# Optimization experiments

Hardware: AMD Instinct MI355X
Metric: run time of the kernel (lower is better)

The kernel has to match this reference:

```python
import jax, jax.numpy as jnp
import numpy as np

B, S, D = 2, 2048, 1024
H, HD = 16, 64          # num_heads, head_dim
K = 32                  # JL n_components


def setup_inputs() -> dict:
    key = jax.random.key(0)
    k1, k2, k3, k4 = jax.random.split(key, 4)
    return {
        "hidden_states": jax.random.normal(k1, (B, S, D), dtype=jnp.float32),
        "W_attn": jax.random.normal(k2, (D, 3 * D), dtype=jnp.float32) * 0.02,
        "b_attn": jnp.zeros((3 * D,), dtype=jnp.float32),
        "S_proj": jax.random.normal(k3, (K, HD), dtype=jnp.float32) / np.sqrt(K),
        "W_proj": jax.random.normal(k4, (D, D), dtype=jnp.float32) * 0.02,
        "b_proj": jnp.zeros((D,), dtype=jnp.float32),
    }


def reference(hidden_states, W_attn, b_attn, S_proj, W_proj, b_proj):
    b, s, d = hidden_states.shape
    # GPT2 Conv1D: x @ W + b, then split into q,k,v
    qkv = hidden_states @ W_attn + b_attn            # [B,S,3D]
    q, k, v = jnp.split(qkv, 3, axis=-1)
    # split heads -> [B,H,S,HD]
    def split_heads(x):
        return x.reshape(b, s, H, HD).transpose(0, 2, 1, 3)
    q = split_heads(q) @ S_proj.T                    # [B,H,S,K] JL-reduced
    k = split_heads(k) @ S_proj.T                    # [B,H,S,K]
    v = split_heads(v)                               # [B,H,S,HD]
    # naive attention: scale by sqrt(value head_dim) per GPT2 _attn
    scores = jnp.einsum("bhqk,bhsk->bhqs", q, k) / jnp.sqrt(
        jnp.asarray(HD, dtype=v.dtype))              # [B,H,S,S]
    causal = jnp.tril(jnp.ones((s, s), dtype=bool))
    mask_value = jnp.finfo(scores.dtype).min
    scores = jnp.where(causal, scores, mask_value)
    attn = jax.nn.softmax(scores, axis=-1)
    out = jnp.einsum("bhqs,bhsd->bhqd", attn, v)     # [B,H,S,HD]
    out = out.transpose(0, 2, 1, 3).reshape(b, s, d)  # merge heads
    return out @ W_proj + b_proj
```

## Files before the change

### kernel.cpp

```cpp
#include <hip/hip_runtime.h>
#include <hip/hip_bf16.h>
#include <stdint.h>

#define B_ 2
#define S_ 2048
#define D_ 1024
#define H_ 16
#define HD_ 64
#define KJL 32
#define N3 3072
#define N2 2048

typedef __attribute__((ext_vector_type(8))) __bf16 bf16x8;
typedef __attribute__((ext_vector_type(4))) float floatx4;
typedef __attribute__((ext_vector_type(4))) short short4v;
typedef __attribute__((ext_vector_type(2))) unsigned int uint2v;

__device__ __forceinline__ unsigned short f2b(float x) {
  union { float f; unsigned u; } v; v.f = x;
  unsigned r = v.u + 0x7fffu + ((v.u >> 16) & 1u);
  return (unsigned short)(r >> 16);
}

__device__ __forceinline__ unsigned int pkbf(float lo, float hi) {
  union { float f; unsigned u; } a, b;
  a.f = lo; b.f = hi;
  return __builtin_amdgcn_perm(b.u + 0x8000u, a.u + 0x8000u, 0x07060302u);
}

__device__ __forceinline__ void async16(const void* g, void* l) {
  __builtin_amdgcn_global_load_lds((__attribute__((address_space(1))) void*)(g),
                                   (__attribute__((address_space(3))) void*)(l),
                                   16, 0, 0);
}

__global__ __launch_bounds__(256)
void prep_kernel(const float* __restrict__ hidden, unsigned short* __restrict__ hB,
                 const float* __restrict__ W_attn, const float* __restrict__ b_attn,
                 const float* __restrict__ Sp, const float* __restrict__ W_proj,
                 unsigned short* __restrict__ Bt2, unsigned short* __restrict__ WpT,
                 float* __restrict__ bias2) {
  __shared__ float shmem[2048];
  const int bid = blockIdx.x;
  const int tid = threadIdx.x;

  if (bid < 512) {
    const int n4 = (B_ * S_ * D_) / 4;
    int i = bid * 256 + tid;
    for (; i < n4; i += 512 * 256) {
      float4 v = *(const float4*)(hidden + 4 * (size_t)i);
      short4v o = {(short)f2b(v.x), (short)f2b(v.y), (short)f2b(v.z), (short)f2b(v.w)};
      *(short4v*)(hB + 4 * (size_t)i) = o;
    }
  } else if (bid < 2560) {
    const float* in;
    unsigned short* out;
    int Cs, local;
    if (bid < 1536) { local = bid - 512;  in = W_attn + 2048; out = Bt2 + 1024 * 1024; Cs = N3; }
    else            { local = bid - 1536; in = W_proj;        out = WpT;               Cs = D_; }
    float (*t)[33] = (float(*)[33])shmem;
    int c0 = (local & 31) * 32, r0 = (local >> 5) * 32;
    int tx = tid & 31, ty = tid >> 5;
    for (int j = 0; j < 32; j += 8)
      t[ty + j][tx] = in[(size_t)(r0 + ty + j) * Cs + c0 + tx];
    __syncthreads();
    for (int j = 0; j < 32; j += 8)
      out[(size_t)(c0 + ty + j) * D_ + r0 + tx] = f2b(t[tx][ty + j]);
  } else {
    const int lb = bid - 2560;
    const int part = lb >> 6;
    const int h = (lb >> 2) & 15;
    const int dc = lb & 3;
    for (int i = tid; i < 32 * 64; i += 256) shmem[i] = Sp[i];
    __syncthreads();
    const float scale = part ? 1.0f : 0.125f * 1.44269504f;
    const int d = dc * 256 + tid;
    float w[64];
    const float* src = W_attn + (size_t)d * N3 + part * D_ + h * 64;
    for (int j = 0; j < 16; ++j) {
      float4 v = *(const float4*)&src[j * 4];
      w[j * 4 + 0] = v.x; w[j * 4 + 1] = v.y; w[j * 4 + 2] = v.z; w[j * 4 + 3] = v.w;
    }
    const int nbase = part * 512 + h * 32;
    for (int kjl = 0; kjl < 32; ++kjl) {
      float acc = 0.f;
      for (int hd = 0; hd < 64; ++hd) acc += w[hd] * shmem[kjl * 64 + hd];
      Bt2[(size_t)(nbase + kjl) * D_ + d] = f2b(acc * scale);
    }
    if (dc == 0 && tid < 32) {
      float acc = 0.f;
      for (int hd = 0; hd < 64; ++hd) acc += b_attn[part * D_ + h * 64 + hd] * shmem[tid * 64 + hd];
      bias2[nbase + tid] = acc * scale;
    }
  }
}

__global__ __launch_bounds__(256, 2)
void qkv2_gemm_kernel(const unsigned short* __restrict__ A,
                      const unsigned short* __restrict__ Bt,
                      const float* __restrict__ b_attn,
                      const float* __restrict__ bias2,
                      unsigned short* __restrict__ Qjl,
                      unsigned short* __restrict__ Kjl,
                      unsigned short* __restrict__ Vc) {
  __shared__ __align__(16) unsigned short As[2][128 * 32];
  __shared__ __align__(16) unsigned short Bs[2][128 * 32];
  const int tid = threadIdx.x;
  const int lane = tid & 63, wv = tid >> 6;
  const int quad = lane >> 4, col = lane & 15;
  const int wm = wv >> 1, wn = wv & 1;
  const int m0 = blockIdx.y * 128, n0 = blockIdx.x * 128;

  floatx4 acc[4][4] = {};

  for (int kk = 0; kk < D_; kk += 64) {
    for (int it = 0; it < 4; ++it) {
      int c = it * 256 + tid;
      int ks = c >> 9, row = (c >> 2) & 127, kc = c & 3;
      async16(A + (size_t)(m0 + row) * D_ + kk + ks * 32 + kc * 8,
              (unsigned short*)As + c * 8);
    }
    for (int it = 0; it < 4; ++it) {
      int c = it * 256 + tid;
      int ks = c >> 9, row = (c >> 2) & 127, kc = c & 3;
      async16(Bt + (size_t)(n0 + row) * D_ + kk + ks * 32 + kc * 8,
              (unsigned short*)Bs + c * 8);
    }
    asm volatile("s_waitcnt vmcnt(0)" ::: "memory");
    __syncthreads();
    for (int ks = 0; ks < 2; ++ks) {
      bf16x8 af[4], bfr[4];
      for (int mt = 0; mt < 4; ++mt)
        af[mt] = *(const bf16x8*)&As[ks][(wm * 64 + mt * 16 + col) * 32 + quad * 8];
      for (int nt = 0; nt < 4; ++nt)
        bfr[nt] = *(const bf16x8*)&Bs[ks][(wn * 64 + nt * 16 + col) * 32 + quad * 8];
      for (int mt = 0; mt < 4; ++mt)
        for (int nt = 0; nt < 4; ++nt)
          acc[mt][nt] = __builtin_amdgcn_mfma_f32_16x16x32_bf16(
              af[mt], bfr[nt], acc[mt][nt], 0, 0, 0);
    }
    __syncthreads();
  }

  const int pq = n0 >> 9;
  for (int mt = 0; mt < 4; ++mt) {
    int gm0 = m0 + wm * 64 + mt * 16 + quad * 4;
    int b = gm0 >> 11, s = gm0 & (S_ - 1);
    for (int nt = 0; nt < 4; ++nt) {
      int gn = n0 + wn * 64 + nt * 16 + col;
      if (pq >= 2) {
        int vcol = gn - 1024;
        float bs = b_attn[2048 + vcol];
        int h = vcol >> 6, hd = vcol & 63;
        short4v vv;
        for (int i = 0; i < 4; ++i)
          vv[i] = (short)f2b(acc[mt][nt][i] + bs);
        size_t idx = ((((size_t)(b * H_ + h) * 64 + (s >> 5)) * 64 + hd) * 32 + (s & 31));
        *(short4v*)&Vc[idx] = vv;
      } else {
        float bs = bias2[gn];
        int gl = gn & 511;
        int h = gl >> 5, kjl = gl & 31;
        unsigned short* dst = pq ? Kjl : Qjl;
        size_t base = ((size_t)(b * H_ + h) * S_ + s) * KJL + kjl;
        for (int i = 0; i < 4; ++i)
          dst[base + (size_t)i * KJL] = f2b(acc[mt][nt][i] + bs);
      }
    }
  }
}

__global__ __launch_bounds__(256, 2)
void attn_kernel(const unsigned short* __restrict__ Qjl,
                 const unsigned short* __restrict__ Kjl,
                 const unsigned short* __restrict__ Vc,
                 unsigned short* __restrict__ AO) {
  __shared__ __align__(16) unsigned short Kb[2][4096];
  __shared__ __align__(16) unsigned short Vb[2][8192];
  __shared__ __align__(16) unsigned short Ps[4][2048];
  const int tid = threadIdx.x;
  const int lane = tid & 63, wv = tid >> 6;
  const int quad = lane >> 4, l15 = lane & 15;

  const int blk = blockIdx.x;
  const int bh = blk & 31;
  const int v = blk >> 5;
  const int b = bh >> 4, h = bh & 15;

  const unsigned short* Kg = Kjl + (size_t)bh * S_ * KJL;
  const unsigned short* Vg = Vc + (size_t)bh * (64 * 64 * 32);

  char* Pw = (char*)&Ps[wv][0];
  const int pswz = l15 << 4;
  const floatx4 zz = {0.f, 0.f, 0.f, 0.f};

#define STAGE(bu, c) do {                                                   \
    const char* ks_ = (const char*)(Kg + (size_t)(c) * 4096);               \
    const char* vs_ = (const char*)(Vg + (size_t)(c) * 8192);               \
    char* kd_ = (char*)&Kb[bu][0];                                          \
    char* vd_ = (char*)&Vb[bu][0];                                          \
    async16(ks_ + tid * 16,         kd_ + tid * 16);                        \
    async16(ks_ + tid * 16 + 4096,  kd_ + tid * 16 + 4096);                 \
    async16(vs_ + tid * 16,         vd_ + tid * 16);                        \
    async16(vs_ + tid * 16 + 4096,  vd_ + tid * 16 + 4096);                 \
    async16(vs_ + tid * 16 + 8192,  vd_ + tid * 16 + 8192);                 \
    async16(vs_ + tid * 16 + 12288, vd_ + tid * 16 + 12288);                \
  } while (0)

  for (int ph = 0; ph < 2; ++ph) {
    const int gv = ph ? (31 - v) : v;
    const int t16 = gv * 4 + wv;
    const int nch = (gv >> 1) + 1;
    const int lastc = nch - 1;
    const int qbase = (gv & 1) * 64 + wv * 16;

    bf16x8 aq = *(const bf16x8*)&Qjl[(size_t)(bh * S_ + t16 * 16 + l15) * KJL + quad * 8];

    floatx4 o[4] = {};
    floatx4 psum = {};

    STAGE(0, 0);
    asm volatile("s_waitcnt vmcnt(0)" ::: "memory");
    __builtin_amdgcn_s_barrier();

    int cur = 0;
    for (int kt = 0; kt < nch; ++kt) {
      if (kt + 1 < nch) STAGE(cur ^ 1, kt + 1);

      const char* Kc = (const char*)&Kb[cur][0];
      const char* Vl = (const char*)&Vb[cur][0];

      bf16x8 ak[8];
      for (int sm = 0; sm < 8; ++sm)
        ak[sm] = *(const bf16x8*)(Kc + (sm * 16 + l15) * 64 + quad * 16);

      floatx4 sc[8];
      __builtin_amdgcn_s_setprio(1);
      for (int sm = 0; sm < 8; ++sm)
        sc[sm] = __builtin_amdgcn_mfma_f32_16x16x32_bf16(ak[sm], aq, zz, 0, 0, 0);
      __builtin_amdgcn_s_setprio(0);

      if (kt == lastc) {
        int qloc = qbase + l15;
        for (int sm = 0; sm < 8; ++sm)
          for (int i = 0; i < 4; ++i)
            if (sm * 16 + quad * 4 + i > qloc) sc[sm][i] = -1e30f;
      }

      for (int sm = 0; sm < 8; ++sm) {
        float p0 = __builtin_amdgcn_exp2f(sc[sm][0]);
        float p1 = __builtin_amdgcn_exp2f(sc[sm][1]);
        float p2 = __builtin_amdgcn_exp2f(sc[sm][2]);
        float p3 = __builtin_amdgcn_exp2f(sc[sm][3]);
        psum[0] += p0; psum[1] += p1; psum[2] += p2; psum[3] += p3;
        uint2v pk2 = {pkbf(p0, p1), pkbf(p2, p3)};
        *(uint2v*)(Pw + l15 * 256 + ((sm * 32 + quad * 8) ^ pswz)) = pk2;
      }

      for (int ks = 0; ks < 4; ++ks) {
        bf16x8 bv[4];
        for (int md = 0; md < 4; ++md)
          bv[md] = *(const bf16x8*)(Vl + ks * 4096 + md * 1024 + l15 * 64 + quad * 16);
        bf16x8 bp = *(const bf16x8*)(Pw + l15 * 256 + ((ks * 64 + quad * 16) ^ pswz));
        __builtin_amdgcn_s_setprio(1);
        for (int md = 0; md < 4; ++md)
          o[md] = __builtin_amdgcn_mfma_f32_16x16x32_bf16(bv[md], bp, o[md], 0, 0, 0);
        __builtin_amdgcn_s_setprio(0);
      }

      asm volatile("s_waitcnt vmcnt(0)" ::: "memory");
      __builtin_amdgcn_s_barrier();
      cur ^= 1;
    }

    float l0 = psum[0] + psum[1] + psum[2] + psum[3];
    l0 += __shfl_xor(l0, 16, 64);
    l0 += __shfl_xor(l0, 32, 64);
    float inv = 1.f / l0;

    {
      const int eswz = (l15 & 7) << 4;
      for (int md = 0; md < 4; ++md) {
        uint2v t4 = {pkbf(o[md][0] * inv, o[md][1] * inv),
                     pkbf(o[md][2] * inv, o[md][3] * inv)};
        *(uint2v*)(Pw + l15 * 128 + ((md * 32 + quad * 8) ^ eswz)) = t4;
      }
      asm volatile("s_waitcnt lgkmcnt(0)" ::: "memory");
      int q = lane >> 2, j = lane & 3;
      size_t gbase = ((size_t)(b * S_ + t16 * 16 + q)) * D_ + h * HD_;
      for (int half = 0; half < 2; ++half) {
        bf16x8 vv = *(const bf16x8*)(Pw + q * 128 + ((half * 64 + j * 16) ^ ((q & 7) << 4)));
        *(bf16x8*)&AO[gbase + half * 32 + j * 8] = vv;
      }
    }
  }
#undef STAGE
}

__global__ __launch_bounds__(256, 2)
void proj_gemm_kernel(const unsigned short* __restrict__ A,
                      const unsigned short* __restrict__ Bt,
                      const float* __restrict__ bias,
                      float* __restrict__ out) {
  __shared__ __align__(16) unsigned short As[2][64 * 32];
  __shared__ __align__(16) unsigned short Bs[2][128 * 32];
  const int tid = threadIdx.x;
  const int lane = tid & 63, wv = tid >> 6;
  const int quad = lane >> 4, col = lane & 15;
  const int wm = wv >> 1, wn = wv & 1;
  const int m0 = blockIdx.y * 64, n0 = blockIdx.x * 128;

  floatx4 acc[2][4] = {};

  for (int kk = 0; kk < D_; kk += 64) {
    for (int it = 0; it < 2; ++it) {
      int c = it * 256 + tid;
      int ks = c >> 8, row = (c >> 2) & 63, kc = c & 3;
      async16(A + (size_t)(m0 + row) * D_ + kk + ks * 32 + kc * 8,
              (unsigned short*)As + c * 8);
    }
    for (int it = 0; it < 4; ++it) {
      int c = it * 256 + tid;
      int ks = c >> 9, row = (c >> 2) & 127, kc = c & 3;
      async16(Bt + (size_t)(n0 + row) * D_ + kk + ks * 32 + kc * 8,
              (unsigned short*)Bs + c * 8);
    }
    asm volatile("s_waitcnt vmcnt(0)" ::: "memory");
    __syncthreads();
    for (int ks = 0; ks < 2; ++ks) {
      bf16x8 af[2], bfr[4];
      for (int mt = 0; mt < 2; ++mt)
        af[mt] = *(const bf16x8*)&As[ks][(wm * 32 + mt * 16 + col) * 32 + quad * 8];
      for (int nt = 0; nt < 4; ++nt)
        bfr[nt] = *(const bf16x8*)&Bs[ks][(wn * 64 + nt * 16 + col) * 32 + quad * 8];
      for (int mt = 0; mt < 2; ++mt)
        for (int nt = 0; nt < 4; ++nt)
          acc[mt][nt] = __builtin_amdgcn_mfma_f32_16x16x32_bf16(
              af[mt], bfr[nt], acc[mt][nt], 0, 0, 0);
    }
    __syncthreads();
  }

  for (int mt = 0; mt < 2; ++mt) {
    int gm0 = m0 + wm * 32 + mt * 16 + quad * 4;
    for (int nt = 0; nt < 4; ++nt) {
      int gn = n0 + wn * 64 + nt * 16 + col;
      float bs = bias[gn];
      for (int i = 0; i < 4; ++i)
        out[(size_t)(gm0 + i) * D_ + gn] = acc[mt][nt][i] + bs;
    }
  }
}

extern "C" void kernel_launch(void* const* d_in, const int* in_sizes, int n_in,
                              void* d_out, int out_size, void* d_ws, size_t ws_size,
                              hipStream_t stream) {
  (void)in_sizes; (void)n_in; (void)out_size; (void)ws_size;
  const float* hidden = (const float*)d_in[0];
  const float* W_attn = (const float*)d_in[1];
  const float* b_attn = (const float*)d_in[2];
  const float* S_proj = (const float*)d_in[3];
  const float* W_proj = (const float*)d_in[4];
  const float* b_proj = (const float*)d_in[5];
  float* out = (float*)d_out;

  char* ws = (char*)d_ws;
  unsigned short* hB    = (unsigned short*)(ws);
  unsigned short* Bt2   = (unsigned short*)(ws + (8u << 20));
  unsigned short* WpT   = (unsigned short*)(ws + (12u << 20));
  float*          bias2 = (float*)         (ws + (14u << 20));
  unsigned short* Qjl   = (unsigned short*)(ws + (15u << 20));
  unsigned short* Kjl   = (unsigned short*)(ws + (19u << 20));
  unsigned short* Vc    = (unsigned short*)(ws + (23u << 20));
  unsigned short* AO    = (unsigned short*)(ws + (31u << 20));

  prep_kernel<<<2688, 256, 0, stream>>>(hidden, hB, W_attn, b_attn, S_proj,
                                        W_proj, Bt2, WpT, bias2);
  qkv2_gemm_kernel<<<dim3(N2 / 128, (B_ * S_) / 128), 256, 0, stream>>>(
      hB, Bt2, b_attn, bias2, Qjl, Kjl, Vc);
  attn_kernel<<<512, 256, 0, stream>>>(Qjl, Kjl, Vc, AO);
  proj_gemm_kernel<<<dim3(D_ / 128, (B_ * S_) / 64), 256, 0, stream>>>(
      AO, WpT, b_proj, out);
}
```

Before: 178.1 us.

## Double-buffer LDS tiles in QKV and projection GEMMs to overlap loads with MFMA

Both GEMM kernels now keep two LDS stages and issue the async global-to-LDS copies for the next K tile before running the MFMAs on the current one. Each iteration then needs only one wait and one barrier instead of a load-wait-compute-barrier sequence, which is meant to hide global memory latency behind compute. It also raises wave priority around the MFMA bursts with s_setprio. The cost is twice the LDS per block (64KB for the QKV kernel), which may limit occupancy at the requested 2 blocks per CU. Dropping the trailing __syncthreads also relies on the s_waitcnt plus s_barrier placement for correctness when a buffer is overwritten.

New measurement: 178.9 us. No clear change (+0.4%).

```diff
diff --git a/kernel.cpp b/kernel.cpp
--- a/kernel.cpp
+++ b/kernel.cpp
@@ -103,8 +103,8 @@
                       unsigned short* __restrict__ Qjl,
                       unsigned short* __restrict__ Kjl,
                       unsigned short* __restrict__ Vc) {
-  __shared__ __align__(16) unsigned short As[2][128 * 32];
-  __shared__ __align__(16) unsigned short Bs[2][128 * 32];
+  __shared__ __align__(16) unsigned short As[2][2 * 128 * 32];
+  __shared__ __align__(16) unsigned short Bs[2][2 * 128 * 32];
   const int tid = threadIdx.x;
   const int lane = tid & 63, wv = tid >> 6;
   const int quad = lane >> 4, col = lane & 15;
@@ -113,34 +113,50 @@
 
   floatx4 acc[4][4] = {};
 
-  for (int kk = 0; kk < D_; kk += 64) {
-    for (int it = 0; it < 4; ++it) {
-      int c = it * 256 + tid;
-      int ks = c >> 9, row = (c >> 2) & 127, kc = c & 3;
-      async16(A + (size_t)(m0 + row) * D_ + kk + ks * 32 + kc * 8,
-              (unsigned short*)As + c * 8);
-    }
-    for (int it = 0; it < 4; ++it) {
-      int c = it * 256 + tid;
-      int ks = c >> 9, row = (c >> 2) & 127, kc = c & 3;
-      async16(Bt + (size_t)(n0 + row) * D_ + kk + ks * 32 + kc * 8,
-              (unsigned short*)Bs + c * 8);
-    }
-    asm volatile("s_waitcnt vmcnt(0)" ::: "memory");
-    __syncthreads();
+#define STAGE_AB(bu, kk) do {                                               \
+    for (int it = 0; it < 4; ++it) {                                        \
+      int c = it * 256 + tid;                                  \
+      int ks = c >> 9, row = (c >> 2) & 127, kc = c & 3;                    \
+      async16(A + (size_t)(m0 + row) * D_ + (kk) + ks * 32 + kc * 8,        \
+              (unsigned short*)As + (bu) * 8192 + c * 8);                   \
+    }                                                                       \
+    for (int it = 0; it < 4; ++it) {                                        \
+      int c = it * 256 + tid;                                               \
+      int ks = c >> 9, row = (c >> 2) & 127, kc = c & 3;                    \
+      async16(Bt + (size_t)(n0 + row) * D_ + (kk) + ks * 32 + kc * 8,       \
+              (unsigned short*)Bs + (bu) * 8192 + c * 8);                   \
+    }                                                                       \
+  } while (0)
+
+  STAGE_AB(0, 0);
+  asm volatile("s_waitcnt vmcnt(0)" ::: "memory");
+  __builtin_amdgcn_s_barrier();
+
+  int buf = 0;
+  for (int kt = 0; kt < 16; ++kt) {
+    if (kt + 1 < 16) STAGE_AB(buf ^ 1, (kt + 1) * 64);
+
+    const unsigned short* Ab = (const unsigned short*)As + buf * 8192;
+    const unsigned short* Bb = (const unsigned short*)Bs + buf * 8192;
     for (int ks = 0; ks < 2; ++ks) {
       bf16x8 af[4], bfr[4];
       for (int mt = 0; mt < 4; ++mt)
-        af[mt] = *(const bf16x8*)&As[ks][(wm * 64 + mt * 16 + col) * 32 + quad * 8];
+        af[mt] = *(const bf16x8*)&Ab[ks * 4096 + (wm * 64 + mt * 16 + col) * 32 + quad * 8];
       for (int nt = 0; nt < 4; ++nt)
-        bfr[nt] = *(const bf16x8*)&Bs[ks][(wn * 64 + nt * 16 + col) * 32 + quad * 8];
+        bfr[nt] = *(const bf16x8*)&Bb[ks * 4096 + (wn * 64 + nt * 16 + col) * 32 + quad * 8];
+      __builtin_amdgcn_s_setprio(1);
       for (int mt = 0; mt < 4; ++mt)
         for (int nt = 0; nt < 4; ++nt)
           acc[mt][nt] = __builtin_amdgcn_mfma_f32_16x16x32_bf16(
               af[mt], bfr[nt], acc[mt][nt], 0, 0, 0);
-    }
-    __syncthreads();
-  }
+      __builtin_amdgcn_s_setprio(0);
+    }
+
+    asm volatile("s_waitcnt vmcnt(0)" ::: "memory");
+    __builtin_amdgcn_s_barrier();
+    buf ^= 1;
+  }
+#undef STAGE_AB
 
   const int pq = n0 >> 9;
   for (int mt = 0; mt < 4; ++mt) {
@@ -302,8 +318,8 @@
                       const unsigned short* __restrict__ Bt,
                       const float* __restrict__ bias,
                       float* __restrict__ out) {
-  __shared__ __align__(16) unsigned short As[2][64 * 32];
-  __shared__ __align__(16) unsigned short Bs[2][128 * 32];
+  __shared__ __align__(16) unsigned short As[2][2 * 64 * 32];
+  __shared__ __align__(16) unsigned short Bs[2][2 * 128 * 32];
   const int tid = threadIdx.x;
   const int lane = tid & 63, wv = tid >> 6;
   const int quad = lane >> 4, col = lane & 15;
@@ -312,34 +328,50 @@
 
   floatx4 acc[2][4] = {};
 
-  for (int kk = 0; kk < D_; kk += 64) {
-    for (int it = 0; it < 2; ++it) {
-      int c = it * 256 + tid;
-      int ks = c >> 8, row = (c >> 2) & 63, kc = c & 3;
-      async16(A + (size_t)(m0 + row) * D_ + kk + ks * 32 + kc * 8,
-              (unsigned short*)As + c * 8);
-    }
-    for (int it = 0; it < 4; ++it) {
-      int c = it * 256 + tid;
-      int ks = c >> 9, row = (c >> 2) & 127, kc = c & 3;
-      async16(Bt + (size_t)(n0 + row) * D_ + kk + ks * 32 + kc * 8,
-              (unsigned short*)Bs + c * 8);
-    }
-    asm volatile("s_waitcnt vmcnt(0)" ::: "memory");
-    __syncthreads();
+#define STAGE_AB(bu, kk) do {                                               \
+    for (int it = 0; it < 2; ++it) {                 \
+      int c = it * 256 + tid;                                               \
+      int ks = c >> 8, row = (c >> 2) & 63, kc = c & 3;                     \
+      async16(A + (size_t)(m0 + row) * D_ + (kk) + ks * 32 + kc * 8,        \
+              (unsigned short*)As + (bu) * 4096 + c * 8);                   \
+    }                                                                       \
+    for (int it = 0; it < 4; ++it) {                \
+      int c = it * 256 + tid;                                               \
+      int ks = c >> 9, row = (c >> 2) & 127, kc = c & 3;                    \
+      async16(Bt + (size_t)(n0 + row) * D_ + (kk) + ks * 32 + kc * 8,       \
+              (unsigned short*)Bs + (bu) * 8192 + c * 8);                   \
+    }                                                                       \
+  } while (0)
+
+  STAGE_AB(0, 0);
+  asm volatile("s_waitcnt vmcnt(0)" ::: "memory");
+  __builtin_amdgcn_s_barrier();
+
+  int buf = 0;
+  for (int kt = 0; kt < 16; ++kt) {
+    if (kt + 1 < 16) STAGE_AB(buf ^ 1, (kt + 1) * 64);
+
+    const unsigned short* Ab = (const unsigned short*)As + buf * 4096;
+    const unsigned short* Bb = (const unsigned short*)Bs + buf * 8192;
     for (int ks = 0; ks < 2; ++ks) {
       bf16x8 af[2], bfr[4];
       for (int mt = 0; mt < 2; ++mt)
-        af[mt] = *(const bf16x8*)&As[ks][(wm * 32 + mt * 16 + col) * 32 + quad * 8];
+        af[mt] = *(const bf16x8*)&Ab[ks * 2048 + (wm * 32 + mt * 16 + col) * 32 + quad * 8];
       for (int nt = 0; nt < 4; ++nt)
-        bfr[nt] = *(const bf16x8*)&Bs[ks][(wn * 64 + nt * 16 + col) * 32 + quad * 8];
+        bfr[nt] = *(const bf16x8*)&Bb[ks * 4096 + (wn * 64 + nt * 16 + col) * 32 + quad * 8];
+      __builtin_amdgcn_s_setprio(1);
       for (int mt = 0; mt < 2; ++mt)
         for (int nt = 0; nt < 4; ++nt)
           acc[mt][nt] = __builtin_amdgcn_mfma_f32_16x16x32_bf16(
               af[mt], bfr[nt], acc[mt][nt], 0, 0, 0);
-    }
-    __syncthreads();
-  }
+      __builtin_amdgcn_s_setprio(0);
+    }
+
+    asm volatile("s_waitcnt vmcnt(0)" ::: "memory");
+    __builtin_amdgcn_s_barrier();
+    buf ^= 1;
+  }
+#undef STAGE_AB
 
   for (int mt = 0; mt < 2; ++mt) {
     int gm0 = m0 + wm * 32 + mt * 16 + quad * 4;
```
